# Kernel optimization log

Measured on AMD Instinct MI355X. Metric: run time of the kernel, lower is better.

## Reference

```python
import jax, jax.numpy as jnp
import numpy as np

B, NUM_TATUMS, F, T = 8, 256, 128, 2048


def repeat_with_tatums(features, tatum_frames, total_frames):
    """Vectorized equivalent of per-sample repeat_interleave + pad_sequence.
    features: (B, num_tatums, F); tatum_frames: (B, num_tatums+1) monotone.
    Frame t of sample i takes tatum j with tatum_frames[i,j] <= t < tatum_frames[i,j+1];
    frames >= tatum_frames[i,-1] are zero padding.
    """
    num_tatums = features.shape[1]
    t = jnp.arange(total_frames)

    def per_sample(f, tf):
        idx = jnp.searchsorted(tf[1:], t, side='right')  # (T,)
        idx = jnp.clip(idx, 0, num_tatums - 1)
        valid = t < tf[-1]
        return jnp.where(valid[:, None], f[idx], jnp.zeros((), f.dtype))

    return jax.vmap(per_sample)(features, tatum_frames)  # (B, T, F)


def conv2d_same(x, w, b):
    y = jax.lax.conv_general_dilated(
        x, w, window_strides=(1, 1), padding='SAME',
        dimension_numbers=('NCHW', 'OIHW', 'NCHW'))
    return y + b[None, :, None, None]


def setup_inputs() -> dict:
    key = jax.random.key(0)
    ks = jax.random.split(key, 12)
    pitch_rendered = jax.random.normal(ks[0], (B, NUM_TATUMS, F), dtype=jnp.float32)
    onset = jax.random.uniform(ks[1], (B, NUM_TATUMS), dtype=jnp.float32)
    tf = jnp.sort(jax.random.randint(ks[2], (B, NUM_TATUMS + 1), 0, T), axis=1)
    tf = tf.at[:, 0].set(0).at[:, -1].set(T)  # boundaries: start 0, end T
    tatum_frames = tf.astype(jnp.int64)
    s = 0.1
    W1 = jax.random.normal(ks[3], (32, 2, 3, 3), dtype=jnp.float32) * s
    b1 = jnp.zeros((32,), jnp.float32)
    W2 = jax.random.normal(ks[4], (32, 32, 3, 3), dtype=jnp.float32) * s
    b2 = jnp.zeros((32,), jnp.float32)
    W3 = jax.random.normal(ks[5], (32, 32, 3, 3), dtype=jnp.float32) * s
    b3 = jnp.zeros((32,), jnp.float32)
    W4 = jax.random.normal(ks[6], (1, 32, 3, 3), dtype=jnp.float32) * s
    b4 = jnp.zeros((1,), jnp.float32)
    return dict(pitch_rendered=pitch_rendered, onset=onset, tatum_frames=tatum_frames,
                W1=W1, b1=b1, W2=W2, b2=b2, W3=W3, b3=b3, W4=W4, b4=b4)


def reference(pitch_rendered, onset, tatum_frames, W1, b1, W2, b2, W3, b3, W4, b4):
    num_features = pitch_rendered.shape[-1]
    pr = repeat_with_tatums(pitch_rendered, tatum_frames, T)            # (B, T, F)
    on = repeat_with_tatums(jnp.broadcast_to(onset[:, :, None], onset.shape + (num_features,)),
                            tatum_frames, T)                             # (B, T, F)
    x = jnp.stack([pr, on], axis=1)                                      # (B, 2, T, F)
    x = jax.nn.relu(conv2d_same(x, W1, b1))
    x = jax.nn.relu(conv2d_same(x, W2, b2))
    x = jax.nn.relu(conv2d_same(x, W3, b3))
    x = conv2d_same(x, W4, b4)                                           # (B, 1, T, F)
    return jnp.squeeze(x, axis=1)                                        # (B, T, F)
```

## Files before the change

kernel.cpp:

```cpp
#include <hip/hip_runtime.h>
#include <hip/hip_bf16.h>

#define TDIM 2048
#define FDIM 128

typedef __attribute__((ext_vector_type(8))) short short8;
typedef __attribute__((ext_vector_type(4))) float f32x4;
typedef __attribute__((ext_vector_type(8))) unsigned short ushort8;

__device__ __forceinline__ unsigned short f2bf(float v) {
    __bf16 h = (__bf16)v;
    return __builtin_bit_cast(unsigned short, h);
}

__global__ void prep_weights_kernel(const float* __restrict__ W1, const float* __restrict__ W2,
                                    const float* __restrict__ W3, const float* __restrict__ W4,
                                    unsigned short* __restrict__ wt)
{
    for (int e = blockIdx.x * 256 + threadIdx.x; e < 26112; e += gridDim.x * 256) {
        float v = 0.0f;
        if (e < 3072) {
            int uv = e >> 8, co = (e >> 3) & 31, ci = e & 7;
            if (uv < 9 && ci < 2) v = W1[co * 18 + ci * 9 + uv];
        } else if (e < 12288) {
            int q = e - 3072;
            int g = q / 2304, r = q % 2304;
            int uv = r >> 8, co = (r >> 3) & 31, ci = g * 8 + (r & 7);
            v = W2[co * 288 + ci * 9 + uv];
        } else if (e < 21504) {
            int q = e - 12288;
            int g = q / 2304, r = q % 2304;
            int uv = r >> 8, co = (r >> 3) & 31, ci = g * 8 + (r & 7);
            v = W3[co * 288 + ci * 9 + uv];
        } else {
            int q = e - 21504;
            int g = q / 1152, r = q % 1152;
            int uv = r >> 7, co = (r >> 3) & 15, ci = g * 8 + (r & 7);
            if (co == 0) v = W4[ci * 9 + uv];
        }
        wt[e] = f2bf(v);
    }
}

__device__ __forceinline__ uint2 pack4(f32x4 c, bool valid) {
    unsigned short h[4];
#pragma unroll
    for (int k = 0; k < 4; ++k) {
        float v = fmaxf(c[k], 0.0f);
        h[k] = valid ? f2bf(v) : (unsigned short)0;
    }
    uint2 r;
    r.x = (unsigned)h[0] | ((unsigned)h[1] << 16);
    r.y = (unsigned)h[2] | ((unsigned)h[3] << 16);
    return r;
}

#define NWAVES 8

template<int WI, int WO, int PSI, int PSO>
__device__ __forceinline__ void conv_mid(const char* __restrict__ inb, char* __restrict__ outb,
                                         const char* __restrict__ wlds, const float* __restrict__ bias,
                                         int wave, int lane, int t_base, int f_base)
{
    const int lm = lane & 15, g = lane >> 4;
    const char* wp = wlds + g * 4608;
    short8 wa0[9], wa1[9];
#pragma unroll
    for (int uv = 0; uv < 9; ++uv) {
        wa0[uv] = *(const short8*)(wp + (uv * 32 + lm) * 16);
        wa1[uv] = *(const short8*)(wp + (uv * 32 + 16 + lm) * 16);
    }
    f32x4 bias0 = *(const f32x4*)(bias + g * 4);
    f32x4 bias1 = *(const f32x4*)(bias + 16 + g * 4);

    const char* inp = inb + g * PSI;
    constexpr int NPX = WO * WO;
    constexpr int NG = (NPX + 15) / 16;
    for (int grp = wave; grp < NG; grp += NWAVES) {
        int m = grp * 16 + lm;
        bool mv = m < NPX;
        int mc = mv ? m : NPX - 1;
        int i = mc / WO, j = mc - i * WO;
        const char* base = inp + (i * WI + j) * 16;
        f32x4 c0 = bias0, c1 = bias1;
#pragma unroll
        for (int u = 0; u < 3; ++u)
#pragma unroll
            for (int v = 0; v < 3; ++v) {
                short8 bf = *(const short8*)(base + (u * WI + v) * 16);
                c0 = __builtin_amdgcn_mfma_f32_16x16x32_bf16(wa0[u * 3 + v], bf, c0, 0, 0, 0);
                c1 = __builtin_amdgcn_mfma_f32_16x16x32_bf16(wa1[u * 3 + v], bf, c1, 0, 0, 0);
            }
        if (mv) {
            int t = t_base + i, f = f_base + j;
            bool valid = (t >= 0) && (t < TDIM) && (f >= 0) && (f < FDIM);
            char* wb = outb + (g >> 1) * PSO + m * 16 + (g & 1) * 8;
            *(uint2*)wb             = pack4(c0, valid);
            *(uint2*)(wb + 2 * PSO) = pack4(c1, valid);
        }
    }
}

__device__ __forceinline__ void conv1_compute(const char* __restrict__ X, const char* __restrict__ w1,
                                              char* __restrict__ Y1, const float* __restrict__ bias,
                                              int wave, int lane, int t_base, int f_base)
{
    const int lm = lane & 15, g = lane >> 4;
    short8 wa0[3], wa1[3];
    int duv[3];
#pragma unroll
    for (int jj = 0; jj < 3; ++jj) {
        int uv = 4 * jj + g;
        wa0[jj] = *(const short8*)(w1 + uv * 512 + lm * 16);
        wa1[jj] = *(const short8*)(w1 + uv * 512 + (16 + lm) * 16);
        int uvc = uv <= 8 ? uv : 0;
        int u = uvc / 3, v = uvc - u * 3;
        duv[jj] = (u * 24 + v) * 16;
    }
    f32x4 bias0 = *(const f32x4*)(bias + g * 4);
    f32x4 bias1 = *(const f32x4*)(bias + 16 + g * 4);

    constexpr int NPX = 22 * 22;
    constexpr int NG = (NPX + 15) / 16;
    for (int grp = wave; grp < NG; grp += NWAVES) {
        int m = grp * 16 + lm;
        bool mv = m < NPX;
        int mc = mv ? m : NPX - 1;
        int i = mc / 22, j = mc - i * 22;
        const char* base = X + (i * 24 + j) * 16;
        f32x4 c0 = bias0, c1 = bias1;
#pragma unroll
        for (int jj = 0; jj < 3; ++jj) {
            short8 bf = *(const short8*)(base + duv[jj]);
            c0 = __builtin_amdgcn_mfma_f32_16x16x32_bf16(wa0[jj], bf, c0, 0, 0, 0);
            c1 = __builtin_amdgcn_mfma_f32_16x16x32_bf16(wa1[jj], bf, c1, 0, 0, 0);
        }
        if (mv) {
            int t = t_base + i, f = f_base + j;
            bool valid = (t >= 0) && (t < TDIM) && (f >= 0) && (f < FDIM);
            char* wb = Y1 + (g >> 1) * 7744 + m * 16 + (g & 1) * 8;
            *(uint2*)wb           = pack4(c0, valid);
            *(uint2*)(wb + 15488) = pack4(c1, valid);
        }
    }
}

__device__ __forceinline__ void conv4_compute(const char* __restrict__ Y3, const char* __restrict__ w4,
                                              const float* __restrict__ b4, float* __restrict__ out,
                                              int wave, int lane, int b, int t0, int f0)
{
    const int lm = lane & 15, g = lane >> 4;
    const char* wp = w4 + g * 2304;
    short8 wa[9];
#pragma unroll
    for (int uv = 0; uv < 9; ++uv)
        wa[uv] = *(const short8*)(wp + (uv * 16 + lm) * 16);
    float bv = b4[0];
    const char* yp = Y3 + g * 5184;
    for (int grp = wave; grp < 16; grp += NWAVES) {
        const char* base = yp + (grp * 18 + lm) * 16;
        f32x4 c = {0.0f, 0.0f, 0.0f, 0.0f};
#pragma unroll
        for (int u = 0; u < 3; ++u)
#pragma unroll
            for (int v = 0; v < 3; ++v) {
                short8 bf = *(const short8*)(base + (u * 18 + v) * 16);
                c = __builtin_amdgcn_mfma_f32_16x16x32_bf16(wa[u * 3 + v], bf, c, 0, 0, 0);
            }
        if (g == 0)
            out[((long)b * TDIM + (t0 + grp)) * FDIM + f0 + lm] = c[0] + bv;
    }
}

__global__ __launch_bounds__(512, 4)
void fused_mfma_kernel(const float* __restrict__ pr, const float* __restrict__ onset,
                       const int* __restrict__ tf,
                       const float* __restrict__ b1, const float* __restrict__ b2,
                       const float* __restrict__ b3, const float* __restrict__ b4,
                       const unsigned short* __restrict__ wt, float* __restrict__ out)
{
    __shared__ __attribute__((aligned(16))) char lds[75008];
    __shared__ int   rowIdx[24];
    __shared__ float rowOnset[24];

    const int tid = threadIdx.x;
    const int lane = tid & 63, wave = tid >> 6;
    const int f0 = blockIdx.x * 16;
    const int t0 = blockIdx.y * 16;
    const int b  = blockIdx.z;

    char* X  = lds;
    char* W1 = lds + 9216;
    char* Y2 = lds;
    char* Y1 = lds + 25600;
    char* Y3 = lds + 25600;
    char* WB = lds + 56576;
    const char* wtb = (const char*)wt;

    if (tid < 24) {
        int t = t0 - 4 + tid;
        int idx = 0; float ons = 0.0f;
        if (t >= 0 && t < TDIM) {
            const int* a = tf + b * 257 + 1;
            int lo = 0, hi = 256;
            while (lo < hi) { int mid = (lo + hi) >> 1; if (a[mid] <= t) lo = mid + 1; else hi = mid; }
            idx = lo < 255 ? lo : 255;
            ons = onset[b * 256 + idx];
        }
        rowIdx[tid] = idx; rowOnset[tid] = ons;
    }
    for (int ch = tid; ch < 384; ch += 512)
        *(short8*)(W1 + ch * 16) = *(const short8*)(wtb + ch * 16);
    for (int ch = tid; ch < 1152; ch += 512)
        *(short8*)(WB + ch * 16) = *(const short8*)(wtb + 6144 + ch * 16);
    __syncthreads();

    for (int p = tid; p < 576; p += 512) {
        int i = p / 24, j = p - (p / 24) * 24;
        int t = t0 - 4 + i, f = f0 - 4 + j;
        float v0 = 0.0f, v1 = 0.0f;
        if (t >= 0 && t < TDIM && f >= 0 && f < FDIM) {
            v0 = pr[(b * 256 + rowIdx[i]) * 128 + f];
            v1 = rowOnset[i];
        }
        ushort8 xv = {f2bf(v0), f2bf(v1), 0, 0, 0, 0, 0, 0};
        *(ushort8*)(X + p * 16) = xv;
    }
    __syncthreads();

    conv1_compute(X, W1, Y1, b1, wave, lane, t0 - 3, f0 - 3);
    __syncthreads();

    conv_mid<22, 20, 7744, 6400>(Y1, Y2, WB, b2, wave, lane, t0 - 2, f0 - 2);
    __syncthreads();

    for (int ch = tid; ch < 1152; ch += 512)
        *(short8*)(WB + ch * 16) = *(const short8*)(wtb + 24576 + ch * 16);
    __syncthreads();

    conv_mid<20, 18, 6400, 5184>(Y2, Y3, WB, b3, wave, lane, t0 - 1, f0 - 1);
    __syncthreads();

    for (int ch = tid; ch < 576; ch += 512)
        *(short8*)(WB + ch * 16) = *(const short8*)(wtb + 43008 + ch * 16);
    __syncthreads();

    conv4_compute(Y3, WB, b4, out, wave, lane, b, t0, f0);
}

extern "C" void kernel_launch(void* const* d_in, const int* in_sizes, int n_in,
                              void* d_out, int out_size, void* d_ws, size_t ws_size,
                              hipStream_t stream) {
    const float* pr    = (const float*)d_in[0];
    const float* onset = (const float*)d_in[1];
    const int*   tf    = (const int*)d_in[2];
    const float* W1 = (const float*)d_in[3];
    const float* B1 = (const float*)d_in[4];
    const float* W2 = (const float*)d_in[5];
    const float* B2 = (const float*)d_in[6];
    const float* W3 = (const float*)d_in[7];
    const float* B3 = (const float*)d_in[8];
    const float* W4 = (const float*)d_in[9];
    const float* B4 = (const float*)d_in[10];
    float* out = (float*)d_out;
    unsigned short* wt = (unsigned short*)d_ws;

    prep_weights_kernel<<<32, 256, 0, stream>>>(W1, W2, W3, W4, wt);
    dim3 grid(FDIM / 16, TDIM / 16, 8);
    fused_mfma_kernel<<<grid, 512, 0, stream>>>(pr, onset, tf, B1, B2, B3, B4, wt, out);
}
```

Baseline: 250.5 us.

## Split interior/edge tiles, repack conv1 K dimension, prefetch weights into registers

The fused kernel becomes a template launched twice: once over interior tiles, where boundary-validity checks are compiled out, and once over the 268 edge tiles per batch with checks kept. Conv1 packs all 9 taps times 2 channels into one 32-wide K slice, so it issues a single MFMA pair per pixel group instead of three. Each pixel now does its own branchless binary search, and later-layer weights are prefetched into registers before the preceding conv so the global load overlaps compute. The 3x3 MFMA chains are also split into two accumulators to shorten dependency chains. The cost is an extra kernel launch, more register pressure, and redundant per-pixel searches over tatum_frames.

```diff
diff --git a/kernel.cpp b/kernel.cpp
--- a/kernel.cpp
+++ b/kernel.cpp
@@ -3,10 +3,11 @@
 
 #define TDIM 2048
 #define FDIM 128
+#define NWAVES 8
 
 typedef __attribute__((ext_vector_type(8))) short short8;
 typedef __attribute__((ext_vector_type(4))) float f32x4;
-typedef __attribute__((ext_vector_type(8))) unsigned short ushort8;
+typedef __attribute__((ext_vector_type(4))) unsigned uint4v;
 
 __device__ __forceinline__ unsigned short f2bf(float v) {
     __bf16 h = (__bf16)v;
@@ -17,23 +18,24 @@
                                     const float* __restrict__ W3, const float* __restrict__ W4,
                                     unsigned short* __restrict__ wt)
 {
-    for (int e = blockIdx.x * 256 + threadIdx.x; e < 26112; e += gridDim.x * 256) {
+    for (int e = blockIdx.x * 256 + threadIdx.x; e < 24064; e += gridDim.x * 256) {
         float v = 0.0f;
-        if (e < 3072) {
-            int uv = e >> 8, co = (e >> 3) & 31, ci = e & 7;
-            if (uv < 9 && ci < 2) v = W1[co * 18 + ci * 9 + uv];
-        } else if (e < 12288) {
-            int q = e - 3072;
+        if (e < 1024) {
+            int cot = e >> 9, kb = (e >> 7) & 3, co16 = (e >> 3) & 15, ee = e & 7;
+            int k = kb * 8 + ee, uv = k >> 1, ch = k & 1, co = cot * 16 + co16;
+            if (uv < 9) v = W1[co * 18 + ch * 9 + uv];
+        } else if (e < 10240) {
+            int q = e - 1024;
             int g = q / 2304, r = q % 2304;
             int uv = r >> 8, co = (r >> 3) & 31, ci = g * 8 + (r & 7);
             v = W2[co * 288 + ci * 9 + uv];
-        } else if (e < 21504) {
-            int q = e - 12288;
+        } else if (e < 19456) {
+            int q = e - 10240;
             int g = q / 2304, r = q % 2304;
             int uv = r >> 8, co = (r >> 3) & 31, ci = g * 8 + (r & 7);
             v = W3[co * 288 + ci * 9 + uv];
         } else {
-            int q = e - 21504;
+            int q = e - 19456;
             int g = q / 1152, r = q % 1152;
             int uv = r >> 7, co = (r >> 3) & 15, ci = g * 8 + (r & 7);
             if (co == 0) v = W4[ci * 9 + uv];
@@ -55,9 +57,7 @@
     return r;
 }
 
-#define NWAVES 8
-
-template<int WI, int WO, int PSI, int PSO>
+template<int WI, int WO, int PSI, int PSO, bool EDGE>
 __device__ __forceinline__ void conv_mid(const char* __restrict__ inb, char* __restrict__ outb,
                                          const char* __restrict__ wlds, const float* __restrict__ bias,
                                          int wave, int lane, int t_base, int f_base)
@@ -72,6 +72,7 @@
     }
     f32x4 bias0 = *(const f32x4*)(bias + g * 4);
     f32x4 bias1 = *(const f32x4*)(bias + 16 + g * 4);
+    const f32x4 zero = {0.0f, 0.0f, 0.0f, 0.0f};
 
     const char* inp = inb + g * PSI;
     constexpr int NPX = WO * WO;
@@ -82,96 +83,33 @@
         int mc = mv ? m : NPX - 1;
         int i = mc / WO, j = mc - i * WO;
         const char* base = inp + (i * WI + j) * 16;
-        f32x4 c0 = bias0, c1 = bias1;
-#pragma unroll
-        for (int u = 0; u < 3; ++u)
-#pragma unroll
-            for (int v = 0; v < 3; ++v) {
-                short8 bf = *(const short8*)(base + (u * WI + v) * 16);
-                c0 = __builtin_amdgcn_mfma_f32_16x16x32_bf16(wa0[u * 3 + v], bf, c0, 0, 0, 0);
-                c1 = __builtin_amdgcn_mfma_f32_16x16x32_bf16(wa1[u * 3 + v], bf, c1, 0, 0, 0);
-            }
+        f32x4 c0a = bias0, c0b = zero, c1a = bias1, c1b = zero;
+#pragma unroll
+        for (int uv = 0; uv < 9; ++uv) {
+            int u = uv / 3, v = uv - u * 3;
+            short8 bf = *(const short8*)(base + (u * WI + v) * 16);
+            if (uv < 5) {
+                c0a = __builtin_amdgcn_mfma_f32_16x16x32_bf16(wa0[uv], bf, c0a, 0, 0, 0);
+                c1a = __builtin_amdgcn_mfma_f32_16x16x32_bf16(wa1[uv], bf, c1a, 0, 0, 0);
+            } else {
+                c0b = __builtin_amdgcn_mfma_f32_16x16x32_bf16(wa0[uv], bf, c0b, 0, 0, 0);
+                c1b = __builtin_amdgcn_mfma_f32_16x16x32_bf16(wa1[uv], bf, c1b, 0, 0, 0);
+            }
+        }
         if (mv) {
-            int t = t_base + i, f = f_base + j;
-            bool valid = (t >= 0) && (t < TDIM) && (f >= 0) && (f < FDIM);
+            bool valid = true;
+            if (EDGE) {
+                int t = t_base + i, f = f_base + j;
+                valid = (t >= 0) && (t < TDIM) && (f >= 0) && (f < FDIM);
+            }
             char* wb = outb + (g >> 1) * PSO + m * 16 + (g & 1) * 8;
-            *(uint2*)wb             = pack4(c0, valid);
-            *(uint2*)(wb + 2 * PSO) = pack4(c1, valid);
-        }
-    }
-}
-
-__device__ __forceinline__ void conv1_compute(const char* __restrict__ X, const char* __restrict__ w1,
-                                              char* __restrict__ Y1, const float* __restrict__ bias,
-                                              int wave, int lane, int t_base, int f_base)
-{
-    const int lm = lane & 15, g = lane >> 4;
-    short8 wa0[3], wa1[3];
-    int duv[3];
-#pragma unroll
-    for (int jj = 0; jj < 3; ++jj) {
-        int uv = 4 * jj + g;
-        wa0[jj] = *(const short8*)(w1 + uv * 512 + lm * 16);
-        wa1[jj] = *(const short8*)(w1 + uv * 512 + (16 + lm) * 16);
-        int uvc = uv <= 8 ? uv : 0;
-        int u = uvc / 3, v = uvc - u * 3;
-        duv[jj] = (u * 24 + v) * 16;
-    }
-    f32x4 bias0 = *(const f32x4*)(bias + g * 4);
-    f32x4 bias1 = *(const f32x4*)(bias + 16 + g * 4);
-
-    constexpr int NPX = 22 * 22;
-    constexpr int NG = (NPX + 15) / 16;
-    for (int grp = wave; grp < NG; grp += NWAVES) {
-        int m = grp * 16 + lm;
-        bool mv = m < NPX;
-        int mc = mv ? m : NPX - 1;
-        int i = mc / 22, j = mc - i * 22;
-        const char* base = X + (i * 24 + j) * 16;
-        f32x4 c0 = bias0, c1 = bias1;
-#pragma unroll
-        for (int jj = 0; jj < 3; ++jj) {
-            short8 bf = *(const short8*)(base + duv[jj]);
-            c0 = __builtin_amdgcn_mfma_f32_16x16x32_bf16(wa0[jj], bf, c0, 0, 0, 0);
-            c1 = __builtin_amdgcn_mfma_f32_16x16x32_bf16(wa1[jj], bf, c1, 0, 0, 0);
-        }
-        if (mv) {
-            int t = t_base + i, f = f_base + j;
-            bool valid = (t >= 0) && (t < TDIM) && (f >= 0) && (f < FDIM);
-            char* wb = Y1 + (g >> 1) * 7744 + m * 16 + (g & 1) * 8;
-            *(uint2*)wb           = pack4(c0, valid);
-            *(uint2*)(wb + 15488) = pack4(c1, valid);
-        }
-    }
-}
-
-__device__ __forceinline__ void conv4_compute(const char* __restrict__ Y3, const char* __restrict__ w4,
-                                              const float* __restrict__ b4, float* __restrict__ out,
-                                              int wave, int lane, int b, int t0, int f0)
-{
-    const int lm = lane & 15, g = lane >> 4;
-    const char* wp = w4 + g * 2304;
-    short8 wa[9];
-#pragma unroll
-    for (int uv = 0; uv < 9; ++uv)
-        wa[uv] = *(const short8*)(wp + (uv * 16 + lm) * 16);
-    float bv = b4[0];
-    const char* yp = Y3 + g * 5184;
-    for (int grp = wave; grp < 16; grp += NWAVES) {
-        const char* base = yp + (grp * 18 + lm) * 16;
-        f32x4 c = {0.0f, 0.0f, 0.0f, 0.0f};
-#pragma unroll
-        for (int u = 0; u < 3; ++u)
-#pragma unroll
-            for (int v = 0; v < 3; ++v) {
-                short8 bf = *(const short8*)(base + (u * 18 + v) * 16);
-                c = __builtin_amdgcn_mfma_f32_16x16x32_bf16(wa[u * 3 + v], bf, c, 0, 0, 0);
-            }
-        if (g == 0)
-            out[((long)b * TDIM + (t0 + grp)) * FDIM + f0 + lm] = c[0] + bv;
-    }
-}
-
+            *(uint2*)wb             = pack4(c0a + c0b, valid);
+            *(uint2*)(wb + 2 * PSO) = pack4(c1a + c1b, valid);
+        }
+    }
+}
+
+template<bool EDGE>
 __global__ __launch_bounds__(512, 4)
 void fused_mfma_kernel(const float* __restrict__ pr, const float* __restrict__ onset,
                        const int* __restrict__ tf,
@@ -179,73 +117,151 @@
                        const float* __restrict__ b3, const float* __restrict__ b4,
                        const unsigned short* __restrict__ wt, float* __restrict__ out)
 {
-    __shared__ __attribute__((aligned(16))) char lds[75008];
-    __shared__ int   rowIdx[24];
-    __shared__ float rowOnset[24];
+    __shared__ __attribute__((aligned(16))) char lds[77312];
 
     const int tid = threadIdx.x;
     const int lane = tid & 63, wave = tid >> 6;
-    const int f0 = blockIdx.x * 16;
-    const int t0 = blockIdx.y * 16;
-    const int b  = blockIdx.z;
-
-    char* X  = lds;
-    char* W1 = lds + 9216;
-    char* Y2 = lds;
-    char* Y1 = lds + 25600;
-    char* Y3 = lds + 25600;
-    char* WB = lds + 56576;
+    int f0, t0;
+    if (EDGE) {
+        int id = blockIdx.x;
+        int bx, by;
+        if (id < 128)      { bx = 0; by = id; }
+        else if (id < 256) { bx = 7; by = id - 128; }
+        else {
+            int q = id - 256;
+            if (q < 6) { bx = 1 + q; by = 0; }
+            else       { bx = 1 + (q - 6); by = 127; }
+        }
+        f0 = bx * 16; t0 = by * 16;
+    } else {
+        f0 = (blockIdx.x + 1) * 16;
+        t0 = (blockIdx.y + 1) * 16;
+    }
+    const int b = blockIdx.z;
+
+    unsigned* X4 = (unsigned*)lds;
+    char* Y2 = lds + 2304;
+    char* Y1 = lds + 27904;
+    char* Y3 = lds + 27904;
+    char* WB = lds + 58880;
     const char* wtb = (const char*)wt;
 
-    if (tid < 24) {
-        int t = t0 - 4 + tid;
-        int idx = 0; float ons = 0.0f;
-        if (t >= 0 && t < TDIM) {
-            const int* a = tf + b * 257 + 1;
-            int lo = 0, hi = 256;
-            while (lo < hi) { int mid = (lo + hi) >> 1; if (a[mid] <= t) lo = mid + 1; else hi = mid; }
-            idx = lo < 255 ? lo : 255;
-            ons = onset[b * 256 + idx];
-        }
-        rowIdx[tid] = idx; rowOnset[tid] = ons;
-    }
-    for (int ch = tid; ch < 384; ch += 512)
-        *(short8*)(W1 + ch * 16) = *(const short8*)(wtb + ch * 16);
     for (int ch = tid; ch < 1152; ch += 512)
-        *(short8*)(WB + ch * 16) = *(const short8*)(wtb + 6144 + ch * 16);
-    __syncthreads();
+        *(short8*)(WB + ch * 16) = *(const short8*)(wtb + 2048 + ch * 16);
 
     for (int p = tid; p < 576; p += 512) {
         int i = p / 24, j = p - (p / 24) * 24;
         int t = t0 - 4 + i, f = f0 - 4 + j;
-        float v0 = 0.0f, v1 = 0.0f;
-        if (t >= 0 && t < TDIM && f >= 0 && f < FDIM) {
-            v0 = pr[(b * 256 + rowIdx[i]) * 128 + f];
-            v1 = rowOnset[i];
-        }
-        ushort8 xv = {f2bf(v0), f2bf(v1), 0, 0, 0, 0, 0, 0};
-        *(ushort8*)(X + p * 16) = xv;
-    }
-    __syncthreads();
-
-    conv1_compute(X, W1, Y1, b1, wave, lane, t0 - 3, f0 - 3);
-    __syncthreads();
-
-    conv_mid<22, 20, 7744, 6400>(Y1, Y2, WB, b2, wave, lane, t0 - 2, f0 - 2);
-    __syncthreads();
-
-    for (int ch = tid; ch < 1152; ch += 512)
-        *(short8*)(WB + ch * 16) = *(const short8*)(wtb + 24576 + ch * 16);
-    __syncthreads();
-
-    conv_mid<20, 18, 6400, 5184>(Y2, Y3, WB, b3, wave, lane, t0 - 1, f0 - 1);
-    __syncthreads();
-
-    for (int ch = tid; ch < 576; ch += 512)
-        *(short8*)(WB + ch * 16) = *(const short8*)(wtb + 43008 + ch * 16);
-    __syncthreads();
-
-    conv4_compute(Y3, WB, b4, out, wave, lane, b, t0, f0);
+        unsigned xv = 0u;
+        bool valid = true;
+        if (EDGE) valid = (t >= 0) && (t < TDIM) && (f >= 0) && (f < FDIM);
+        if (valid) {
+            const int* a = tf + b * 257 + 1;
+            int pos = 0;
+#pragma unroll
+            for (int step = 128; step >= 1; step >>= 1) {
+                pos += (a[pos + step - 1] <= t) ? step : 0;
+            }
+            int idx = pos < 255 ? pos : 255;
+            float v0 = pr[(b * 256 + idx) * 128 + f];
+            float v1 = onset[b * 256 + idx];
+            xv = (unsigned)f2bf(v0) | ((unsigned)f2bf(v1) << 16);
+        }
+        X4[p] = xv;
+    }
+    __syncthreads();
+
+    const int lm = lane & 15, g = lane >> 4;
+
+    {
+        const short8 waA = *(const short8*)(wtb + (g * 16 + lm) * 16);
+        const short8 waB = *(const short8*)(wtb + (64 + g * 16 + lm) * 16);
+        int off4[4];
+#pragma unroll
+        for (int q = 0; q < 4; ++q) {
+            int uv = g * 4 + q;
+            int uvc = uv <= 8 ? uv : 8;
+            int u = uvc / 3, v = uvc - u * 3;
+            off4[q] = u * 24 + v;
+        }
+        f32x4 bias0 = *(const f32x4*)(b1 + g * 4);
+        f32x4 bias1 = *(const f32x4*)(b1 + 16 + g * 4);
+
+        constexpr int NPX = 22 * 22;
+        constexpr int NG = (NPX + 15) / 16;
+        for (int grp = wave; grp < NG; grp += NWAVES) {
+            int m = grp * 16 + lm;
+            bool mv = m < NPX;
+            int mc = mv ? m : NPX - 1;
+            int i = mc / 22, j = mc - i * 22;
+            int base4 = i * 24 + j;
+            uint4v bu;
+#pragma unroll
+            for (int q = 0; q < 4; ++q) bu[q] = X4[base4 + off4[q]];
+            short8 bf = __builtin_bit_cast(short8, bu);
+            f32x4 c0 = __builtin_amdgcn_mfma_f32_16x16x32_bf16(waA, bf, bias0, 0, 0, 0);
+            f32x4 c1 = __builtin_amdgcn_mfma_f32_16x16x32_bf16(waB, bf, bias1, 0, 0, 0);
+            if (mv) {
+                bool valid = true;
+                if (EDGE) {
+                    int t = t0 - 3 + i, f = f0 - 3 + j;
+                    valid = (t >= 0) && (t < TDIM) && (f >= 0) && (f < FDIM);
+                }
+                char* wb = Y1 + (g >> 1) * 7744 + m * 16 + (g & 1) * 8;
+                *(uint2*)wb           = pack4(c0, valid);
+                *(uint2*)(wb + 15488) = pack4(c1, valid);
+            }
+        }
+    }
+
+    short8 w3p0 = *(const short8*)(wtb + 20480 + tid * 16);
+    short8 w3p1 = *(const short8*)(wtb + 20480 + (tid + 512) * 16);
+    short8 w3p2;
+    if (tid < 128) w3p2 = *(const short8*)(wtb + 20480 + (tid + 1024) * 16);
+    __syncthreads();
+
+    conv_mid<22, 20, 7744, 6400, EDGE>(Y1, Y2, WB, b2, wave, lane, t0 - 2, f0 - 2);
+    __syncthreads();
+
+    *(short8*)(WB + tid * 16) = w3p0;
+    *(short8*)(WB + (tid + 512) * 16) = w3p1;
+    if (tid < 128) *(short8*)(WB + (tid + 1024) * 16) = w3p2;
+    __syncthreads();
+
+    short8 w4p0 = *(const short8*)(wtb + 38912 + tid * 16);
+    short8 w4p1;
+    if (tid < 64) w4p1 = *(const short8*)(wtb + 38912 + (tid + 512) * 16);
+
+    conv_mid<20, 18, 6400, 5184, EDGE>(Y2, Y3, WB, b3, wave, lane, t0 - 1, f0 - 1);
+    __syncthreads();
+
+    *(short8*)(WB + tid * 16) = w4p0;
+    if (tid < 64) *(short8*)(WB + (tid + 512) * 16) = w4p1;
+    __syncthreads();
+
+    {
+        const char* wp = WB + g * 2304;
+        short8 wa[9];
+#pragma unroll
+        for (int uv = 0; uv < 9; ++uv)
+            wa[uv] = *(const short8*)(wp + (uv * 16 + lm) * 16);
+        float bv = b4[0];
+        const char* yp = Y3 + g * 5184;
+        const f32x4 zero = {0.0f, 0.0f, 0.0f, 0.0f};
+        for (int grp = wave; grp < 16; grp += NWAVES) {
+            const char* base = yp + (grp * 18 + lm) * 16;
+            f32x4 ca = zero, cb = zero;
+#pragma unroll
+            for (int uv = 0; uv < 9; ++uv) {
+                int u = uv / 3, v = uv - u * 3;
+                short8 bf = *(const short8*)(base + (u * 18 + v) * 16);
+                if (uv < 5) ca = __builtin_amdgcn_mfma_f32_16x16x32_bf16(wa[uv], bf, ca, 0, 0, 0);
+                else        cb = __builtin_amdgcn_mfma_f32_16x16x32_bf16(wa[uv], bf, cb, 0, 0, 0);
+            }
+            if (g == 0)
+                out[((long)b * TDIM + (t0 + grp)) * FDIM + f0 + lm] = ca[0] + cb[0] + bv;
+        }
+    }
 }
 
 extern "C" void kernel_launch(void* const* d_in, const int* in_sizes, int n_in,
@@ -266,6 +282,10 @@
     unsigned short* wt = (unsigned short*)d_ws;
 
     prep_weights_kernel<<<32, 256, 0, stream>>>(W1, W2, W3, W4, wt);
-    dim3 grid(FDIM / 16, TDIM / 16, 8);
-    fused_mfma_kernel<<<grid, 512, 0, stream>>>(pr, onset, tf, B1, B2, B3, B4, wt, out);
-}
+
+    dim3 gridI(6, 126, 8);
+    fused_mfma_kernel<false><<<gridI, 512, 0, stream>>>(pr, onset, tf, B1, B2, B3, B4, wt, out);
+
+    dim3 gridE(268, 1, 8);
+    fused_mfma_kernel<true><<<gridE, 512, 0, stream>>>(pr, onset, tf, B1, B2, B3, B4, wt, out);
+}
```

Result: no change. 251.6 us (+0.4%).
